# Kernel tuning notes

Measured on AMD Instinct MI355X. Metric: run time of the kernel, lower is better.

## Reference

```python
import jax, jax.numpy as jnp
import numpy as np

N_NODES = 100000
N_EDGES = 1600000
N_FEAT = 64
HIDDEN = 16


def setup_inputs() -> dict:
    key = jax.random.key(0)
    ks = jax.random.split(key, 10)
    x = jax.random.normal(ks[0], (N_NODES, N_FEAT), dtype=jnp.float32)
    edge_index = jax.random.randint(ks[1], (2, N_EDGES), 0, N_NODES, dtype=jnp.int64)
    As = jax.random.normal(ks[2], (2, N_EDGES), dtype=jnp.float32)
    ws_weights = jax.random.normal(ks[3], (2,), dtype=jnp.float32)
    Wl1 = jax.random.normal(ks[4], (N_FEAT, HIDDEN), dtype=jnp.float32) / np.sqrt(N_FEAT)
    bl1 = jnp.zeros((HIDDEN,), dtype=jnp.float32)
    Wr1 = jax.random.normal(ks[5], (N_FEAT, HIDDEN), dtype=jnp.float32) / np.sqrt(N_FEAT)
    Wl2 = jax.random.normal(ks[6], (HIDDEN, 1), dtype=jnp.float32) / np.sqrt(HIDDEN)
    bl2 = jnp.zeros((1,), dtype=jnp.float32)
    Wr2 = jax.random.normal(ks[7], (HIDDEN, 1), dtype=jnp.float32) / np.sqrt(HIDDEN)
    return {"x": x, "edge_index": edge_index, "As": As, "ws_weights": ws_weights,
            "Wl1": Wl1, "bl1": bl1, "Wr1": Wr1, "Wl2": Wl2, "bl2": bl2, "Wr2": Wr2}


def reference(x, edge_index, As, ws_weights, Wl1, bl1, Wr1, Wl2, bl2, Wr2):
    # WeightedSumLayer: weighted sum of per-edge weight vectors
    ewm = jnp.einsum('m,me->e', ws_weights, As)  # [E]
    # edge mask (nonzero weighted sum keeps the edge); instead of slicing to a
    # data-dependent edge count, zero out masked messages (same aggregation).
    mask = (ewm != 0).astype(x.dtype)  # [E]
    src, dst = edge_index[0], edge_index[1]
    n = x.shape[0]

    # SAGEConv layer 1 (aggr='sum'): out = lin_l(sum_j x_j) + lin_r(x)
    msg1 = x[src] * mask[:, None]                             # [E, F]
    agg1 = jax.ops.segment_sum(msg1, dst, num_segments=n)     # [N, F]
    h = jax.nn.relu(agg1 @ Wl1 + bl1 + x @ Wr1)               # [N, H]

    # SAGEConv layer 2
    msg2 = h[src] * mask[:, None]                             # [E, H]
    agg2 = jax.ops.segment_sum(msg2, dst, num_segments=n)     # [N, H]
    out = agg2 @ Wl2 + bl2 + h @ Wr2                          # [N, 1]
    return out
```

## Files before the change

### kernel.cpp

```cpp
#include <hip/hip_runtime.h>
#include <hip/hip_bf16.h>

constexpr int NN = 100000;
constexpr int NE = 1600000;
constexpr int NF = 64;
constexpr int NH = 16;

constexpr int NPB  = 128;
constexpr int LB   = 7;
constexpr int NBKT = (NN + NPB - 1) / NPB;
constexpr int CAP  = 2560;
constexpr int CHUNK = 4096;
constexpr int NBLK_B  = (NE + CHUNK - 1) / CHUNK;
constexpr int NBLK_K1 = (NN + 255) / 256;

constexpr int SMEM_BYTES = (CHUNK * 2 + 2 * NBKT * 4) > (2 * NF * NH * 4)
                         ? (CHUNK * 2 + 2 * NBKT * 4) : (2 * NF * NH * 4);

__device__ __forceinline__ float bf16_to_f32(unsigned short u) {
    return __uint_as_float(((unsigned int)u) << 16);
}
__device__ __forceinline__ unsigned short f32_to_bf16(float f) {
    __hip_bfloat16 hb = __float2bfloat16(f);
    return *reinterpret_cast<unsigned short*>(&hb);
}

__global__ __launch_bounds__(256)
void k_fused(const float* __restrict__ x,
             const float* __restrict__ Wl1,
             const float* __restrict__ Wr1,
             unsigned short* __restrict__ p,
             float* __restrict__ r,
             const int* __restrict__ ei, const float* __restrict__ As,
             const float* __restrict__ ws,
             int* __restrict__ bcnt, unsigned int* __restrict__ bmem)
{
    __shared__ __align__(16) char smem[SMEM_BYTES];
    int role = blockIdx.x & 1;
    int rb   = blockIdx.x >> 1;
    int tid  = threadIdx.x;

    if (role == 0) {
        float* sW = (float*)smem;
        for (int i = tid; i < NF * NH; i += 256) {
            sW[i]           = Wl1[i];
            sW[NF * NH + i] = Wr1[i];
        }
        __syncthreads();

        int n = rb * 256 + tid;
        if (n >= NN) return;

        float aL[NH], aR[NH];
#pragma unroll
        for (int j = 0; j < NH; ++j) { aL[j] = 0.f; aR[j] = 0.f; }

        const float4* xr = reinterpret_cast<const float4*>(x + (size_t)n * NF);
#pragma unroll
        for (int k4 = 0; k4 < NF / 4; ++k4) {
            float4 v = xr[k4];
            float xs[4] = {v.x, v.y, v.z, v.w};
#pragma unroll
            for (int t = 0; t < 4; ++t) {
                const float* wl = &sW[(k4 * 4 + t) * NH];
                const float* wr = &sW[NF * NH + (k4 * 4 + t) * NH];
#pragma unroll
                for (int j = 0; j < NH; ++j) {
                    aL[j] = fmaf(xs[t], wl[j], aL[j]);
                    aR[j] = fmaf(xs[t], wr[j], aR[j]);
                }
            }
        }

        unsigned int pu[8];
#pragma unroll
        for (int j2 = 0; j2 < 8; ++j2)
            pu[j2] = (unsigned int)f32_to_bf16(aL[2*j2]) |
                     ((unsigned int)f32_to_bf16(aL[2*j2+1]) << 16);
        uint4* pp = reinterpret_cast<uint4*>(p + (size_t)n * NH);
        pp[0] = make_uint4(pu[0], pu[1], pu[2], pu[3]);
        pp[1] = make_uint4(pu[4], pu[5], pu[6], pu[7]);

        float4* rp = reinterpret_cast<float4*>(r + (size_t)n * NH);
#pragma unroll
        for (int j4 = 0; j4 < NH / 4; ++j4)
            rp[j4] = make_float4(aR[j4*4], aR[j4*4+1], aR[j4*4+2], aR[j4*4+3]);
    } else {
        unsigned short* srk = (unsigned short*)smem;
        int* lcnt  = (int*)(smem + CHUNK * 2);
        int* lbase = lcnt + NBKT;

        for (int i = tid; i < NBKT; i += 256) lcnt[i] = 0;
        __syncthreads();

        int base = rb * CHUNK;
        float w0 = ws[0], w1 = ws[1];

#pragma unroll
        for (int j = 0; j < CHUNK / 256; ++j) {
            int idx = j * 256 + tid;
            int e = base + idx;
            unsigned short rk = 0xFFFFu;
            if (e < NE) {
                float ewm = w0 * As[e] + w1 * As[NE + e];
                if (ewm != 0.f)
                    rk = (unsigned short)atomicAdd(&lcnt[ei[NE + e] >> LB], 1);
            }
            srk[idx] = rk;
        }
        __syncthreads();

        for (int i = tid; i < NBKT; i += 256) {
            int c = lcnt[i];
            lbase[i] = c ? atomicAdd(&bcnt[i], c) : 0;
        }
        __syncthreads();

#pragma unroll
        for (int j = 0; j < CHUNK / 256; ++j) {
            int idx = j * 256 + tid;
            unsigned short rk = srk[idx];
            if (rk != 0xFFFFu) {
                int e   = base + idx;
                int dst = ei[NE + e];
                int bk  = dst >> LB;
                int slot = lbase[bk] + rk;
                if (slot < CAP)
                    bmem[(size_t)bk * CAP + slot] =
                        ((unsigned)ei[e] << LB) | (unsigned)(dst & (NPB - 1));
            }
        }
    }
}

__global__ __launch_bounds__(256)
void k_agg1(const int* __restrict__ bcnt, unsigned int* __restrict__ bmem,
            const unsigned short* __restrict__ p, const float* __restrict__ r,
            const float* __restrict__ bl1, const float* __restrict__ Wl2,
            const float* __restrict__ bl2, const float* __restrict__ Wr2,
            float* __restrict__ q, float* __restrict__ out,
            int* __restrict__ gsoff)
{
    __shared__ unsigned int sbm[CAP];
    __shared__ unsigned int ssorted[CAP];
    __shared__ int hist[NPB];
    __shared__ int scan[NPB];
    __shared__ int soff[NPB + 1];

    int b = blockIdx.x;
    int tid = threadIdx.x;
    if (tid < NPB) hist[tid] = 0;
    __syncthreads();

    int cnt = min(bcnt[b], CAP);

    int rk[CAP / 256];
#pragma unroll
    for (int j = 0; j < CAP / 256; ++j) {
        int i = j * 256 + tid;
        if (i < cnt) {
            unsigned int w = bmem[(size_t)b * CAP + i];
            sbm[i] = w;
            rk[j] = atomicAdd(&hist[w & (NPB - 1)], 1);
        }
    }
    __syncthreads();

    if (tid < NPB) scan[tid] = hist[tid];
    __syncthreads();
    for (int off = 1; off < NPB; off <<= 1) {
        int u = (tid < NPB && tid >= off) ? scan[tid - off] : 0;
        __syncthreads();
        if (tid < NPB) scan[tid] += u;
        __syncthreads();
    }
    if (tid < NPB) soff[tid + 1] = scan[tid];
    if (tid == 0) soff[0] = 0;
    __syncthreads();

#pragma unroll
    for (int j = 0; j < CAP / 256; ++j) {
        int i = j * 256 + tid;
        if (i < cnt) {
            unsigned int w = sbm[i];
            ssorted[soff[w & (NPB - 1)] + rk[j]] = w;
        }
    }
    __syncthreads();

    for (int i = tid; i < cnt; i += 256)
        bmem[(size_t)b * CAP + i] = ssorted[i];
    if (tid < NPB + 1)
        gsoff[(size_t)b * (NPB + 1) + tid] = soff[tid];

    int g = tid >> 4, k = tid & 15;
    int n0 = b * NPB;
#pragma unroll
    for (int jj = 0; jj < 8; ++jj) {
        int nl = g * 8 + jj;
        int s = soff[nl], e = soff[nl + 1];
        float a = 0.f;
        int i = s;
        for (; i + 3 < e; i += 4) {
            unsigned w0 = ssorted[i], w1 = ssorted[i+1], w2 = ssorted[i+2], w3 = ssorted[i+3];
            float v0 = bf16_to_f32(p[(size_t)(w0 >> LB) * NH + k]);
            float v1 = bf16_to_f32(p[(size_t)(w1 >> LB) * NH + k]);
            float v2 = bf16_to_f32(p[(size_t)(w2 >> LB) * NH + k]);
            float v3 = bf16_to_f32(p[(size_t)(w3 >> LB) * NH + k]);
            a += (v0 + v1) + (v2 + v3);
        }
        for (; i < e; ++i)
            a += bf16_to_f32(p[(size_t)(ssorted[i] >> LB) * NH + k]);

        int n = n0 + nl;
        if (n < NN) {
            float h = a + r[(size_t)n * NH + k] + bl1[k];
            h = h > 0.f ? h : 0.f;
            float qv = h * Wl2[k];
            float sv = h * Wr2[k];
#pragma unroll
            for (int m = 8; m >= 1; m >>= 1) {
                qv += __shfl_xor(qv, m);
                sv += __shfl_xor(sv, m);
            }
            if (k == 0) {
                q[n]   = qv;
                out[n] = sv + bl2[0];
            }
        }
    }
}

__global__ __launch_bounds__(256)
void k_agg2(const int* __restrict__ gsoff, const unsigned int* __restrict__ bmem,
            const float* __restrict__ q, float* __restrict__ out)
{
    int n = blockIdx.x * 256 + threadIdx.x;
    if (n >= NN) return;
    int b  = n >> LB;
    int dl = n & (NPB - 1);
    int s = gsoff[(size_t)b * (NPB + 1) + dl];
    int e = gsoff[(size_t)b * (NPB + 1) + dl + 1];
    const unsigned int* bm = bmem + (size_t)b * CAP;

    float a = 0.f;
    int i = s;
    for (; i + 3 < e; i += 4) {
        unsigned w0 = bm[i], w1 = bm[i+1], w2 = bm[i+2], w3 = bm[i+3];
        a += (q[w0 >> LB] + q[w1 >> LB]) + (q[w2 >> LB] + q[w3 >> LB]);
    }
    for (; i < e; ++i)
        a += q[bm[i] >> LB];
    out[n] += a;
}

extern "C" void kernel_launch(void* const* d_in, const int* in_sizes, int n_in,
                              void* d_out, int out_size, void* d_ws, size_t ws_size,
                              hipStream_t stream)
{
    const float* x   = (const float*)d_in[0];
    const int*   ei  = (const int*)  d_in[1];
    const float* As  = (const float*)d_in[2];
    const float* ws  = (const float*)d_in[3];
    const float* Wl1 = (const float*)d_in[4];
    const float* bl1 = (const float*)d_in[5];
    const float* Wr1 = (const float*)d_in[6];
    const float* Wl2 = (const float*)d_in[7];
    const float* bl2 = (const float*)d_in[8];
    const float* Wr2 = (const float*)d_in[9];
    float* out = (float*)d_out;

    unsigned short* p     = (unsigned short*)d_ws;
    float*          r     = (float*)(p + (size_t)NN * NH);
    float*          q     = r + (size_t)NN * NH;
    int*            bcnt  = (int*)(q + NN);
    int*            gsoff = bcnt + NBKT;
    unsigned int*   bmem  = (unsigned int*)(gsoff + (size_t)NBKT * (NPB + 1));

    hipMemsetAsync(bcnt, 0, NBKT * sizeof(int), stream);

    int nblk = 2 * ((NBLK_B > NBLK_K1) ? NBLK_B : NBLK_K1);
    k_fused<<<nblk, 256, 0, stream>>>(x, Wl1, Wr1, p, r, ei, As, ws, bcnt, bmem);
    k_agg1<<<NBKT, 256, 0, stream>>>(bcnt, bmem, p, r, bl1, Wl2, bl2, Wr2, q, out, gsoff);
    k_agg2<<<(NN + 255) / 256, 256, 0, stream>>>(gsoff, bmem, q, out);
}
```

Baseline: 178.7 us.

## Replace global atomic bucket scatter with per-chunk sorted segments and directory

The edge-binning stage no longer uses global atomics on per-bucket counters to scatter into bucket slots. Each chunk block now does a local scan and writes its edges, grouped by bucket, contiguously into its own chunk buffer, plus a per-chunk offset directory. The aggregation kernel gathers each bucket's segments from all chunks using a scan over the directory, which also removes the memset launch. The gather costs roughly 391 small strided directory reads per bucket, and the per-chunk writes become coalesced.

```diff
diff --git a/kernel.cpp b/kernel.cpp
--- a/kernel.cpp
+++ b/kernel.cpp
@@ -11,11 +11,11 @@
 constexpr int NBKT = (NN + NPB - 1) / NPB;
 constexpr int CAP  = 2560;
 constexpr int CHUNK = 4096;
-constexpr int NBLK_B  = (NE + CHUNK - 1) / CHUNK;
+constexpr int NBF   = (NE + CHUNK - 1) / CHUNK;
 constexpr int NBLK_K1 = (NN + 255) / 256;
-
-constexpr int SMEM_BYTES = (CHUNK * 2 + 2 * NBKT * 4) > (2 * NF * NH * 4)
-                         ? (CHUNK * 2 + 2 * NBKT * 4) : (2 * NF * NH * 4);
+constexpr int FD = NBKT + 1;
+
+constexpr int SMEM_BYTES = CHUNK * 4 + CHUNK * 4 + NBKT * 4 + FD * 4 + 256 * 4;
 
 __device__ __forceinline__ float bf16_to_f32(unsigned short u) {
     return __uint_as_float(((unsigned int)u) << 16);
@@ -33,7 +33,7 @@
              float* __restrict__ r,
              const int* __restrict__ ei, const float* __restrict__ As,
              const float* __restrict__ ws,
-             int* __restrict__ bcnt, unsigned int* __restrict__ bmem)
+             unsigned int* __restrict__ gchunk, int* __restrict__ fdir)
 {
     __shared__ __align__(16) char smem[SMEM_BYTES];
     int role = blockIdx.x & 1;
@@ -86,9 +86,11 @@
         for (int j4 = 0; j4 < NH / 4; ++j4)
             rp[j4] = make_float4(aR[j4*4], aR[j4*4+1], aR[j4*4+2], aR[j4*4+3]);
     } else {
-        unsigned short* srk = (unsigned short*)smem;
-        int* lcnt  = (int*)(smem + CHUNK * 2);
-        int* lbase = lcnt + NBKT;
+        unsigned int* sw    = (unsigned int*)smem;
+        unsigned int* srk   = sw + CHUNK;
+        int*          lcnt  = (int*)(srk + CHUNK);
+        int*          fscan = lcnt + NBKT;
+        int*          tscan = fscan + FD;
 
         for (int i = tid; i < NBKT; i += 256) lcnt[i] = 0;
         __syncthreads();
@@ -100,41 +102,66 @@
         for (int j = 0; j < CHUNK / 256; ++j) {
             int idx = j * 256 + tid;
             int e = base + idx;
-            unsigned short rk = 0xFFFFu;
+            unsigned int rk = 0xFFFFFFFFu, w = 0;
             if (e < NE) {
                 float ewm = w0 * As[e] + w1 * As[NE + e];
-                if (ewm != 0.f)
-                    rk = (unsigned short)atomicAdd(&lcnt[ei[NE + e] >> LB], 1);
-            }
+                if (ewm != 0.f) {
+                    int dst = ei[NE + e];
+                    int bk  = dst >> LB;
+                    w  = ((unsigned)ei[e] << LB) | (unsigned)(dst & (NPB - 1));
+                    int rank = atomicAdd(&lcnt[bk], 1);
+                    rk = ((unsigned)bk << 12) | (unsigned)rank;
+                }
+            }
+            sw[idx]  = w;
             srk[idx] = rk;
         }
         __syncthreads();
 
-        for (int i = tid; i < NBKT; i += 256) {
-            int c = lcnt[i];
-            lbase[i] = c ? atomicAdd(&bcnt[i], c) : 0;
-        }
-        __syncthreads();
+        {
+            int loc[4]; int s = 0;
+#pragma unroll
+            for (int g = 0; g < 4; ++g) {
+                int idx = tid * 4 + g;
+                int v = (idx < NBKT) ? lcnt[idx] : 0;
+                loc[g] = s; s += v;
+            }
+            tscan[tid] = s;
+            __syncthreads();
+            for (int off = 1; off < 256; off <<= 1) {
+                int u = (tid >= off) ? tscan[tid - off] : 0;
+                __syncthreads();
+                tscan[tid] += u;
+                __syncthreads();
+            }
+            int bse = (tid > 0) ? tscan[tid - 1] : 0;
+#pragma unroll
+            for (int g = 0; g < 4; ++g) {
+                int idx = tid * 4 + g;
+                if (idx < NBKT) fscan[idx] = bse + loc[g];
+            }
+            if (tid == 255) fscan[NBKT] = tscan[255];
+        }
+        __syncthreads();
+
+        for (int i = tid; i < FD; i += 256)
+            fdir[(size_t)rb * FD + i] = fscan[i];
 
 #pragma unroll
         for (int j = 0; j < CHUNK / 256; ++j) {
             int idx = j * 256 + tid;
-            unsigned short rk = srk[idx];
-            if (rk != 0xFFFFu) {
-                int e   = base + idx;
-                int dst = ei[NE + e];
-                int bk  = dst >> LB;
-                int slot = lbase[bk] + rk;
-                if (slot < CAP)
-                    bmem[(size_t)bk * CAP + slot] =
-                        ((unsigned)ei[e] << LB) | (unsigned)(dst & (NPB - 1));
+            unsigned int rk = srk[idx];
+            if (rk != 0xFFFFFFFFu) {
+                int pos = fscan[rk >> 12] + (int)(rk & 4095u);
+                gchunk[(size_t)rb * CHUNK + pos] = sw[idx];
             }
         }
     }
 }
 
 __global__ __launch_bounds__(256)
-void k_agg1(const int* __restrict__ bcnt, unsigned int* __restrict__ bmem,
+void k_agg1(const int* __restrict__ fdir, const unsigned int* __restrict__ gchunk,
+            unsigned int* __restrict__ bmem,
             const unsigned short* __restrict__ p, const float* __restrict__ r,
             const float* __restrict__ bl1, const float* __restrict__ Wl2,
             const float* __restrict__ bl2, const float* __restrict__ Wr2,
@@ -143,38 +170,83 @@
 {
     __shared__ unsigned int sbm[CAP];
     __shared__ unsigned int ssorted[CAP];
+    __shared__ int fstart[NBF];
+    __shared__ int foff[NBF + 1];
+    __shared__ int tscan[256];
     __shared__ int hist[NPB];
-    __shared__ int scan[NPB];
+    __shared__ int hscan[NPB];
     __shared__ int soff[NPB + 1];
 
     int b = blockIdx.x;
     int tid = threadIdx.x;
     if (tid < NPB) hist[tid] = 0;
-    __syncthreads();
-
-    int cnt = min(bcnt[b], CAP);
+
+    {
+        int loc[2]; int s = 0;
+#pragma unroll
+        for (int g = 0; g < 2; ++g) {
+            int f = tid * 2 + g;
+            int sz = 0;
+            if (f < NBF) {
+                int s0 = fdir[(size_t)f * FD + b];
+                int s1 = fdir[(size_t)f * FD + b + 1];
+                fstart[f] = s0;
+                sz = s1 - s0;
+            }
+            loc[g] = s; s += sz;
+        }
+        tscan[tid] = s;
+        __syncthreads();
+        for (int off = 1; off < 256; off <<= 1) {
+            int u = (tid >= off) ? tscan[tid - off] : 0;
+            __syncthreads();
+            tscan[tid] += u;
+            __syncthreads();
+        }
+        int bse = (tid > 0) ? tscan[tid - 1] : 0;
+#pragma unroll
+        for (int g = 0; g < 2; ++g) {
+            int f = tid * 2 + g;
+            if (f < NBF) foff[f] = bse + loc[g];
+        }
+        if (tid == 255) foff[NBF] = tscan[255];
+    }
+    __syncthreads();
+
+    int cnt = min(foff[NBF], CAP);
+
+    {
+        int grp = tid >> 4, k = tid & 15;
+        for (int f = grp; f < NBF; f += 16) {
+            int o  = foff[f];
+            int sz = foff[f + 1] - o;
+            int s  = fstart[f];
+            const unsigned int* src = gchunk + (size_t)f * CHUNK + s;
+            int lim = min(sz, CAP - o);
+            for (int j = k; j < lim; j += 16)
+                sbm[o + j] = src[j];
+        }
+    }
+    __syncthreads();
 
     int rk[CAP / 256];
 #pragma unroll
     for (int j = 0; j < CAP / 256; ++j) {
         int i = j * 256 + tid;
-        if (i < cnt) {
-            unsigned int w = bmem[(size_t)b * CAP + i];
-            sbm[i] = w;
-            rk[j] = atomicAdd(&hist[w & (NPB - 1)], 1);
-        }
-    }
-    __syncthreads();
-
-    if (tid < NPB) scan[tid] = hist[tid];
+        if (i < cnt)
+            rk[j] = atomicAdd(&hist[sbm[i] & (NPB - 1)], 1);
+    }
+    __syncthreads();
+
+    if (tid < NPB) hscan[tid] = hist[tid];
     __syncthreads();
     for (int off = 1; off < NPB; off <<= 1) {
-        int u = (tid < NPB && tid >= off) ? scan[tid - off] : 0;
-        __syncthreads();
-        if (tid < NPB) scan[tid] += u;
-        __syncthreads();
-    }
-    if (tid < NPB) soff[tid + 1] = scan[tid];
+        int u = (tid < NPB && tid >= off) ? hscan[tid - off] : 0;
+        __syncthreads();
+        if (tid < NPB) hscan[tid] += u;
+        __syncthreads();
+    }
+    if (tid < NPB) soff[tid + 1] = hscan[tid];
     if (tid == 0) soff[0] = 0;
     __syncthreads();
 
@@ -270,17 +342,17 @@
     const float* Wr2 = (const float*)d_in[9];
     float* out = (float*)d_out;
 
-    unsigned short* p     = (unsigned short*)d_ws;
-    float*          r     = (float*)(p + (size_t)NN * NH);
-    float*          q     = r + (size_t)NN * NH;
-    int*            bcnt  = (int*)(q + NN);
-    int*            gsoff = bcnt + NBKT;
-    unsigned int*   bmem  = (unsigned int*)(gsoff + (size_t)NBKT * (NPB + 1));
-
-    hipMemsetAsync(bcnt, 0, NBKT * sizeof(int), stream);
-
-    int nblk = 2 * ((NBLK_B > NBLK_K1) ? NBLK_B : NBLK_K1);
-    k_fused<<<nblk, 256, 0, stream>>>(x, Wl1, Wr1, p, r, ei, As, ws, bcnt, bmem);
-    k_agg1<<<NBKT, 256, 0, stream>>>(bcnt, bmem, p, r, bl1, Wl2, bl2, Wr2, q, out, gsoff);
+    unsigned short* p      = (unsigned short*)d_ws;
+    float*          r      = (float*)(p + (size_t)NN * NH);
+    float*          q      = r + (size_t)NN * NH;
+    int*            gsoff  = (int*)(q + NN);
+    int*            fdir   = gsoff + (size_t)NBKT * (NPB + 1);
+    unsigned int*   gchunk = (unsigned int*)(fdir + (size_t)NBF * FD);
+    unsigned int*   bmem   = gchunk + (size_t)NBF * CHUNK;
+
+    int nblk = 2 * ((NBF > NBLK_K1) ? NBF : NBLK_K1);
+    k_fused<<<nblk, 256, 0, stream>>>(x, Wl1, Wr1, p, r, ei, As, ws, gchunk, fdir);
+    k_agg1<<<NBKT, 256, 0, stream>>>(fdir, gchunk, bmem, p, r, bl1, Wl2, bl2, Wr2,
+                                     q, out, gsoff);
     k_agg2<<<(NN + 255) / 256, 256, 0, stream>>>(gsoff, bmem, q, out);
 }
```

Measured after the change: 181.7 us. No clear change (+1.7%).
